# Performance work log

Measured on AMD Instinct MI355X. Metric: run time of the kernel, lower is better.

The kernel has to match this reference:

```python
import jax, jax.numpy as jnp
import numpy as np

MID = 16
HEADS = 8
HEAD_DIM = MID // HEADS  # 2
EPS = 1e-5


def posembed(length, dim):
    # get_posembed_linear: sin-cos 1D positional embedding
    pos = jnp.arange(length, dtype=jnp.float32)
    omega = jnp.arange(dim // 2, dtype=jnp.float32) / (dim / 2.0)
    omega = 1.0 / (10000.0 ** omega)
    out = pos[:, None] * omega[None, :]  # [L, dim//2]
    return jnp.concatenate([jnp.sin(out), jnp.cos(out)], axis=1)  # [L, dim]


def layernorm(x, g, b):
    m = x.mean(-1, keepdims=True)
    v = ((x - m) ** 2).mean(-1, keepdims=True)
    return (x - m) * jax.lax.rsqrt(v + EPS) * g + b


def conv2d(x, w, b):
    # NCHW 3x3 SAME conv
    y = jax.lax.conv_general_dilated(x, w, (1, 1), 'SAME',
                                     dimension_numbers=('NCHW', 'OIHW', 'NCHW'))
    return y + b[None, :, None, None]


def attention(x, wq, wk, wv, wo, bo):
    # diffusers Attention: self-attn, no qkv bias, out bias
    B, S, C = x.shape
    q = (x @ wq.T).reshape(B, S, HEADS, HEAD_DIM)
    k = (x @ wk.T).reshape(B, S, HEADS, HEAD_DIM)
    v = (x @ wv.T).reshape(B, S, HEADS, HEAD_DIM)
    scale = 1.0 / np.sqrt(HEAD_DIM).astype(np.float32)
    scores = jnp.einsum('bshd,bthd->bhst', q, k) * scale
    p = jax.nn.softmax(scores, axis=-1)
    o = jnp.einsum('bhst,bthd->bshd', p, v).reshape(B, S, C)
    return o @ wo.T + bo


def setup_inputs() -> dict:
    key = jax.random.key(0)
    ks = jax.random.split(key, 24)

    def n(k, shape, s=0.05):
        return jax.random.normal(k, shape, dtype=jnp.float32) * s

    b, f, h, w, c = 2, 16, 64, 64, 16
    inp = {
        'hidden_states': n(ks[0], (b, f, h, w, c), 1.0),
        'ref_stats': n(ks[1], (b, f, h, w, c), 1.0),
        'emb': n(ks[2], (b, 512), 1.0),
        'conv_in_w': n(ks[3], (MID, c, 3, 3)),
        'conv_in_b': jnp.zeros((MID,), jnp.float32),
        'emb1_w': n(ks[4], (MID, 512)),
        'emb1_b': jnp.zeros((MID,), jnp.float32),
        'emb2_w': n(ks[5], (MID, MID)),
        'emb2_b': jnp.zeros((MID,), jnp.float32),
        'wqx': n(ks[6], (MID, MID)), 'wkx': n(ks[7], (MID, MID)),
        'wvx': n(ks[8], (MID, MID)), 'wox': n(ks[9], (MID, MID)),
        'box': jnp.zeros((MID,), jnp.float32),
        'wqy': n(ks[10], (MID, MID)), 'wky': n(ks[11], (MID, MID)),
        'wvy': n(ks[12], (MID, MID)), 'woy': n(ks[13], (MID, MID)),
        'boy': jnp.zeros((MID,), jnp.float32),
        'wqt': n(ks[14], (MID, MID)), 'wkt': n(ks[15], (MID, MID)),
        'wvt': n(ks[16], (MID, MID)), 'wot': n(ks[17], (MID, MID)),
        'bot': jnp.zeros((MID,), jnp.float32),
        'norm_g': jnp.ones((MID,), jnp.float32),
        'norm_b': jnp.zeros((MID,), jnp.float32),
        'proj_w': n(ks[18], (c, MID, 3, 3)),  # zero_module in torch; random here so grads flow
        'proj_b': jnp.zeros((c,), jnp.float32),
    }
    return inp


def reference(hidden_states, ref_stats, emb,
              conv_in_w, conv_in_b, emb1_w, emb1_b, emb2_w, emb2_b,
              wqx, wkx, wvx, wox, box,
              wqy, wky, wvy, woy, boy,
              wqt, wkt, wvt, wot, bot,
              norm_g, norm_b, proj_w, proj_b):
    b, f, h, w, c = hidden_states.shape

    # conv stem on (b f) c h w
    x = hidden_states.reshape(b * f, h, w, c).transpose(0, 3, 1, 2)
    x = conv2d(x, conv_in_w, conv_in_b)
    r = ref_stats.reshape(b * f, h, w, c).transpose(0, 3, 1, 2)
    r = conv2d(r, conv_in_w, conv_in_b)

    # TimestepEmbedding: linear -> silu -> linear, broadcast over frames/HW
    e = jax.nn.silu(emb @ emb1_w.T + emb1_b) @ emb2_w.T + emb2_b  # [b, MID]
    r = r + jnp.repeat(e, f, axis=0)[:, :, None, None]

    hs = x.reshape(b, f, MID, h, w).transpose(0, 1, 3, 4, 2)  # b f h w c
    rs = r.reshape(b, f, MID, h, w).transpose(0, 1, 3, 4, 2)

    # row (x) attention: cat along w -> (b f h) 2w c
    cat = jnp.concatenate([hs, rs], axis=3).reshape(b * f * h, 2 * w, MID)
    pe = posembed(2 * w, MID)
    resx = attention(layernorm(cat + pe[None], norm_g, norm_b), wqx, wkx, wvx, wox, box)
    resx = resx[:, :w].reshape(b, f, h, w, MID)

    # column (y) attention: cat along h -> (b f w) 2h c
    cat = jnp.concatenate([resx, rs], axis=2)            # b f 2h w c
    cat = cat.transpose(0, 1, 3, 2, 4).reshape(b * f * w, 2 * h, MID)
    pe = posembed(2 * h, MID)
    resy = attention(layernorm(cat + pe[None], norm_g, norm_b), wqy, wky, wvy, woy, boy)
    resy = resy[:, :h].reshape(b, f, w, h, MID).transpose(0, 1, 3, 2, 4)

    # temporal (t) attention: cat along f -> (b h w) 2f c
    cat = jnp.concatenate([resy, rs], axis=1)            # b 2f h w c
    cat = cat.transpose(0, 2, 3, 1, 4).reshape(b * h * w, 2 * f, MID)
    pe = posembed(2 * f, MID)
    rest = attention(layernorm(cat + pe[None], norm_g, norm_b), wqt, wkt, wvt, wot, bot)
    rest = rest[:, :f].reshape(b, h, w, f, MID).transpose(0, 3, 4, 1, 2).reshape(b * f, MID, h, w)

    out = conv2d(rest, proj_w, proj_b)  # (b f) c h w
    return hidden_states + out.reshape(b, f, c, h, w).transpose(0, 1, 3, 4, 2)
```

## Files before the change

kernel.cpp:

```cpp
#include <hip/hip_runtime.h>
#include <hip/hip_bf16.h>

typedef __hip_bfloat16 bf16;
using hf2 = decltype(__builtin_amdgcn_cvt_pkrtz(0.f, 0.f));
typedef float f32x2 __attribute__((ext_vector_type(2)));

#define BB   2
#define FF   16
#define HH   64
#define WW   64
#define CC   16
#define NIMG (BB*FF)
#define PIX  (HH*WW)
#define IMGSZ (PIX*CC)

#define QSCALE_LOG2E 1.0201394f

__device__ __forceinline__ unsigned pkh2(float a, float b) {
    union { hf2 h; unsigned u; } x;
    x.h = __builtin_amdgcn_cvt_pkrtz(a, b);
    return x.u;
}
__device__ __forceinline__ float fdot2u(unsigned a, unsigned b, float c) {
    union { unsigned u; hf2 h; } A, B;
    A.u = a; B.u = b;
    return __builtin_amdgcn_fdot2(A.h, B.h, c, false);
}
__device__ __forceinline__ f32x2 f2(float a, float b) {
    f32x2 r; r.x = a; r.y = b; return r;
}

__device__ __forceinline__ void ld16bf(const bf16* p, float* x) {
    const uint4* p4 = reinterpret_cast<const uint4*>(p);
    uint4 u0 = p4[0], u1 = p4[1];
    unsigned uu[8] = {u0.x, u0.y, u0.z, u0.w, u1.x, u1.y, u1.z, u1.w};
    #pragma unroll
    for (int k = 0; k < 8; ++k) {
        union { unsigned u; float f; } lo, hi;
        lo.u = uu[k] << 16;
        hi.u = uu[k] & 0xffff0000u;
        x[2 * k] = lo.f;
        x[2 * k + 1] = hi.f;
    }
}
__device__ __forceinline__ void st16bf(bf16* p, const float* x) {
    union { bf16 h[16]; uint4 u[2]; } o;
    #pragma unroll
    for (int k = 0; k < 16; ++k) o.h[k] = __float2bfloat16(x[k]);
    uint4* p4 = reinterpret_cast<uint4*>(p);
    p4[0] = o.u[0];
    p4[1] = o.u[1];
}

__device__ __forceinline__ void ld16f(const float* p, float* x) {
    const float4* p4 = reinterpret_cast<const float4*>(p);
    #pragma unroll
    for (int q = 0; q < 4; ++q) {
        float4 v = p4[q];
        x[4 * q] = v.x; x[4 * q + 1] = v.y; x[4 * q + 2] = v.z; x[4 * q + 3] = v.w;
    }
}
__device__ __forceinline__ void st16f(float* p, const float* x) {
    float4* p4 = reinterpret_cast<float4*>(p);
    #pragma unroll
    for (int q = 0; q < 4; ++q)
        p4[q] = make_float4(x[4 * q], x[4 * q + 1], x[4 * q + 2], x[4 * q + 3]);
}

__device__ __forceinline__ unsigned packbf2(float a, float b) {
    union { bf16 h[2]; unsigned u; } pk;
    pk.h[0] = __float2bfloat16(a);
    pk.h[1] = __float2bfloat16(b);
    return pk.u;
}

__global__ __launch_bounds__(256) void conv_in_kernel(
    const float* __restrict__ hid, const float* __restrict__ ref,
    const float* __restrict__ cw, const float* __restrict__ cb,
    const float* __restrict__ emb,
    const float* __restrict__ e1w, const float* __restrict__ e1b,
    const float* __restrict__ e2w, const float* __restrict__ e2b,
    bf16* __restrict__ A, bf16* __restrict__ R)
{
    __shared__ unsigned w2l[9 * 128];
    __shared__ float bl[16], hl[16], el[16];
    __shared__ __align__(16) unsigned stg[6 * 64 * 10];

    int t = threadIdx.x;
    if (t < 128) {
        int oc = t & 15, c2 = t >> 4;
        #pragma unroll
        for (int k = 0; k < 9; ++k)
            w2l[k * 128 + oc * 8 + c2] =
                pkh2(cw[(oc * 16 + 2 * c2) * 9 + k],
                     cw[(oc * 16 + 2 * c2 + 1) * 9 + k]);
    }
    if (t < 16) bl[t] = cb[t];

    int gid  = blockIdx.x * 256 + t;
    int wi   = gid & 63;
    int hi   = (gid >> 6) & 63;
    int r0   = hi & ~3;
    int img2 = gid >> 12;
    int isref = img2 >> 5;
    int img  = img2 & 31;
    int bi   = img >> 4;

    if (isref) {
        float* red = reinterpret_cast<float*>(stg);
        {
            int o = t >> 4, seg = t & 15;
            const float* er = emb + bi * 512 + seg * 32;
            const float* wr = e1w + o * 512 + seg * 32;
            float p = 0.f;
            #pragma unroll
            for (int k = 0; k < 32; ++k) p = fmaf(er[k], wr[k], p);
            red[t] = p;
        }
        __syncthreads();
        if (t < 16) {
            float acc = e1b[t];
            #pragma unroll
            for (int s = 0; s < 16; ++s) acc += red[t * 16 + s];
            hl[t] = acc / (1.f + __expf(-acc));
        }
        __syncthreads();
        if (t < 16) {
            float acc = e2b[t];
            #pragma unroll
            for (int k = 0; k < 16; ++k) acc = fmaf(hl[k], e2w[t * 16 + k], acc);
            el[t] = acc;
        }
        __syncthreads();
    }

    const float* inp = (isref ? ref : hid) + (size_t)img * IMGSZ;
    #pragma unroll
    for (int pass = 0; pass < 2; ++pass) {
        int s = t + pass * 256;
        if (s < 384) {
            int px = s & 63, rr = s >> 6;
            int y  = r0 - 1 + rr;
            if ((unsigned)y < 64u) {
                float xv[16];
                ld16f(inp + (((y << 6) + px) << 4), xv);
                uint2* dst = reinterpret_cast<uint2*>(&stg[(rr * 64 + px) * 10]);
                #pragma unroll
                for (int e = 0; e < 4; ++e)
                    dst[e] = make_uint2(pkh2(xv[4 * e],     xv[4 * e + 1]),
                                        pkh2(xv[4 * e + 2], xv[4 * e + 3]));
            }
        }
    }
    __syncthreads();

    int rb = hi & 3;
    float acc[16];
    #pragma unroll
    for (int oc = 0; oc < 16; ++oc)
        acc[oc] = bl[oc] + (isref ? el[oc] : 0.f);

    #pragma unroll
    for (int ky = 0; ky < 3; ++ky) {
        int y = hi + ky - 1;
        if ((unsigned)y >= 64u) continue;
        int rr = rb + ky;
        #pragma unroll
        for (int kx = 0; kx < 3; ++kx) {
            int xx = wi + kx - 1;
            if ((unsigned)xx >= 64u) continue;
            const uint2* pp = reinterpret_cast<const uint2*>(&stg[(rr * 64 + xx) * 10]);
            uint2 p0 = pp[0], p1 = pp[1], p2 = pp[2], p3 = pp[3];
            unsigned xp[8] = {p0.x, p0.y, p1.x, p1.y, p2.x, p2.y, p3.x, p3.y};
            const unsigned* wt = &w2l[(ky * 3 + kx) * 128];
            #pragma unroll
            for (int oc = 0; oc < 16; ++oc) {
                float a = acc[oc];
                #pragma unroll
                for (int c2 = 0; c2 < 8; ++c2)
                    a = fdot2u(xp[c2], wt[oc * 8 + c2], a);
                acc[oc] = a;
            }
        }
    }
    bf16* op = (isref ? R : A) + ((size_t)(img * PIX + (hi << 6) + wi) << 4);
    st16bf(op, acc);
}

template<int S, int SEQPB, int MINW, bool F16OUT>
__global__ __launch_bounds__(256, MINW) void attn_kernel(
    bf16* __restrict__ A, const bf16* __restrict__ R,
    unsigned* __restrict__ A16,
    int d2, int str1, int str2, int tokStride,
    const float* __restrict__ wq, const float* __restrict__ wk,
    const float* __restrict__ wv, const float* __restrict__ wo,
    const float* __restrict__ bo, const float* __restrict__ gw,
    const float* __restrict__ bw)
{
    constexpr int HS  = S / 2;
    constexpr int KQ  = S / 2;
    constexpr int TPT = 256 / (SEQPB * S);
    constexpr int ITEMS = 256 / SEQPB;
    constexpr int NQG = ITEMS / 16;
    constexpr int QB  = HS / NQG;
    constexpr int QP  = QB / 2;
    constexpr int KROW = 10;
    constexpr int QROW = 20;
    constexpr int LSQ = (SEQPB == 1) ? 0 : ((SEQPB == 2) ? 1 : 2);
    constexpr int NW3 = SEQPB * HS * 8 / 256;

    __shared__ float wolT[256];
    __shared__ unsigned wq2L[128], wk2L[128], wv2L[128];
    __shared__ float bol[16], gl[16], blw[16];
    __shared__ __align__(16) unsigned kU[SEQPB * S * KROW];
    __shared__ __align__(16) unsigned vU[SEQPB * S * KROW];
    __shared__ __align__(16) unsigned qL[SEQPB * HS * KROW];
    __shared__ int bases[SEQPB];

    int t = threadIdx.x;
    wolT[(t & 15) * 16 + (t >> 4)] = wo[t];
    if (t < 128) {
        float2 qw = reinterpret_cast<const float2*>(wq)[t];
        float2 kw = reinterpret_cast<const float2*>(wk)[t];
        float2 vw = reinterpret_cast<const float2*>(wv)[t];
        wq2L[t] = pkh2(qw.x * QSCALE_LOG2E, qw.y * QSCALE_LOG2E);
        wk2L[t] = pkh2(kw.x, kw.y);
        wv2L[t] = pkh2(vw.x, vw.y);
    }
    if (t < 16) { bol[t] = bo[t]; gl[t] = gw[t]; blw[t] = bw[t]; }
    if (t < SEQPB) {
        int seq = blockIdx.x * SEQPB + t;
        bases[t] = (seq / d2) * str1 + (seq % d2) * str2;
    }
    __syncthreads();

    const float om[8] = {1.f, 0.31622776601683794f, 0.1f, 0.031622776601683794f,
                         0.01f, 0.0031622776601683794f, 0.001f, 0.00031622776601683794f};

    if constexpr (TPT == 2) {
        int tokIdx = t >> 1;
        int half = t & 1;
        int db   = half * 8;
        int sq = tokIdx & (SEQPB - 1);
        int i  = tokIdx >> LSQ;
        const bf16* src = ((i < HS)
            ? (A + bases[sq] + (size_t)i * tokStride)
            : (R + bases[sq] + (size_t)(i - HS) * tokStride)) + db;
        uint4 u = *reinterpret_cast<const uint4*>(src);
        unsigned uu[4] = {u.x, u.y, u.z, u.w};
        float x[8];
        #pragma unroll
        for (int k = 0; k < 4; ++k) {
            union { unsigned u; float f; } lo, hi2;
            lo.u = uu[k] << 16; hi2.u = uu[k] & 0xffff0000u;
            x[2 * k] = lo.f; x[2 * k + 1] = hi2.f;
        }
        float fi = (float)i;
        #pragma unroll
        for (int k = 0; k < 8; ++k) {
            float sv, cv;
            __sincosf(fi * om[k], &sv, &cv);
            x[k] += half ? cv : sv;
        }
        float s8 = 0.f;
        #pragma unroll
        for (int k = 0; k < 8; ++k) s8 += x[k];
        float m = (s8 + __shfl_xor(s8, 1)) * (1.f / 16.f);
        float v8 = 0.f;
        #pragma unroll
        for (int k = 0; k < 8; ++k) { float d = x[k] - m; v8 = fmaf(d, d, v8); }
        float var = (v8 + __shfl_xor(v8, 1)) * (1.f / 16.f);
        float rs = rsqrtf(var + 1e-5f);

        unsigned xpm[4];
        #pragma unroll
        for (int e = 0; e < 4; ++e) {
            float a0 = (x[2 * e]     - m) * rs * gl[db + 2 * e]     + blw[db + 2 * e];
            float a1 = (x[2 * e + 1] - m) * rs * gl[db + 2 * e + 1] + blw[db + 2 * e + 1];
            xpm[e] = pkh2(a0, a1);
        }
        unsigned xp[8];
        #pragma unroll
        for (int e = 0; e < 4; ++e) {
            unsigned oth = __shfl_xor(xpm[e], 1);
            xp[e]     = half ? oth    : xpm[e];
            xp[e + 4] = half ? xpm[e] : oth;
        }
        float qv[8], kv[8], vv[8];
        #pragma unroll
        for (int dd = 0; dd < 8; ++dd) {
            int d = db + dd;
            float aq = 0.f, ak = 0.f, av = 0.f;
            #pragma unroll
            for (int c2 = 0; c2 < 8; ++c2) {
                aq = fdot2u(xp[c2], wq2L[d * 8 + c2], aq);
                ak = fdot2u(xp[c2], wk2L[d * 8 + c2], ak);
                av = fdot2u(xp[c2], wv2L[d * 8 + c2], av);
            }
            qv[dd] = aq; kv[dd] = ak; vv[dd] = av;
        }
        int row = (sq * S + i) * KROW + (db >> 1);
        uint2* kr = reinterpret_cast<uint2*>(&kU[row]);
        uint2* vr = reinterpret_cast<uint2*>(&vU[row]);
        #pragma unroll
        for (int e = 0; e < 2; ++e) {
            kr[e] = make_uint2(pkh2(kv[4 * e], kv[4 * e + 1]),
                               pkh2(kv[4 * e + 2], kv[4 * e + 3]));
            vr[e] = make_uint2(packbf2(vv[4 * e], vv[4 * e + 1]),
                               packbf2(vv[4 * e + 2], vv[4 * e + 3]));
        }
        if (i < HS) {
            uint2* qr = reinterpret_cast<uint2*>(&qL[(sq * HS + i) * KROW + (db >> 1)]);
            #pragma unroll
            for (int e = 0; e < 2; ++e)
                qr[e] = make_uint2(pkh2(qv[4 * e], qv[4 * e + 1]),
                                   pkh2(qv[4 * e + 2], qv[4 * e + 3]));
        }
    } else {
        int sq = t & (SEQPB - 1);
        int i  = t >> LSQ;
        const bf16* src = (i < HS)
            ? (A + bases[sq] + (size_t)i * tokStride)
            : (R + bases[sq] + (size_t)(i - HS) * tokStride);
        float x[16];
        ld16bf(src, x);
        float fi = (float)i;
        #pragma unroll
        for (int k = 0; k < 8; ++k) {
            float sv, cv;
            __sincosf(fi * om[k], &sv, &cv);
            x[k]     += sv;
            x[k + 8] += cv;
        }
        float m = 0.f;
        #pragma unroll
        for (int c = 0; c < 16; ++c) m += x[c];
        m *= (1.f / 16.f);
        float var = 0.f;
        #pragma unroll
        for (int c = 0; c < 16; ++c) { float d = x[c] - m; var = fmaf(d, d, var); }
        var *= (1.f / 16.f);
        float rs = rsqrtf(var + 1e-5f);
        float xn[16];
        #pragma unroll
        for (int c = 0; c < 16; ++c) xn[c] = (x[c] - m) * rs * gl[c] + blw[c];

        unsigned xp[8];
        #pragma unroll
        for (int c2 = 0; c2 < 8; ++c2) xp[c2] = pkh2(xn[2 * c2], xn[2 * c2 + 1]);

        float qv[16], kv[16], vv[16];
        #pragma unroll
        for (int dd = 0; dd < 16; ++dd) {
            float aq = 0.f, ak = 0.f, av = 0.f;
            #pragma unroll
            for (int c2 = 0; c2 < 8; ++c2) {
                aq = fdot2u(xp[c2], wq2L[dd * 8 + c2], aq);
                ak = fdot2u(xp[c2], wk2L[dd * 8 + c2], ak);
                av = fdot2u(xp[c2], wv2L[dd * 8 + c2], av);
            }
            qv[dd] = aq; kv[dd] = ak; vv[dd] = av;
        }
        int row = (sq * S + i) * KROW;
        uint2* kr = reinterpret_cast<uint2*>(&kU[row]);
        uint2* vr = reinterpret_cast<uint2*>(&vU[row]);
        #pragma unroll
        for (int e = 0; e < 4; ++e) {
            kr[e] = make_uint2(pkh2(kv[4 * e], kv[4 * e + 1]),
                               pkh2(kv[4 * e + 2], kv[4 * e + 3]));
            vr[e] = make_uint2(packbf2(vv[4 * e], vv[4 * e + 1]),
                               packbf2(vv[4 * e + 2], vv[4 * e + 3]));
        }
        if (i < HS) {
            uint2* qr = reinterpret_cast<uint2*>(&qL[(sq * HS + i) * KROW]);
            #pragma unroll
            for (int e = 0; e < 4; ++e)
                qr[e] = make_uint2(pkh2(qv[4 * e], qv[4 * e + 1]),
                                   pkh2(qv[4 * e + 2], qv[4 * e + 3]));
        }
    }
    __syncthreads();

    int sq2 = t / ITEMS;
    int r   = t % ITEMS;
    int qg  = r >> 4;
    int hd  = (r >> 1) & 7;
    int half2 = r & 1;
    float* oL = reinterpret_cast<float*>(kU);
    {
        unsigned q2[QB];
        f32x2 l2[QP], a0p[QP], a1p[QP];
        #pragma unroll
        for (int qq = 0; qq < QB; ++qq)
            q2[qq] = qL[(sq2 * HS + qg * QB + qq) * KROW + hd];
        #pragma unroll
        for (int m = 0; m < QP; ++m) {
            l2[m] = f2(0.f, 0.f); a0p[m] = f2(0.f, 0.f); a1p[m] = f2(0.f, 0.f);
        }
        const unsigned* kp = &kU[(sq2 * S + half2) * KROW + hd];
        const unsigned* vp = &vU[(sq2 * S + half2) * KROW + hd];
        #pragma unroll 8
        for (int jj = 0; jj < KQ; ++jj) {
            unsigned ku = kp[jj * 2 * KROW];
            unsigned vu = vp[jj * 2 * KROW];
            union { unsigned u; float f; } v0, v1;
            v0.u = vu << 16; v1.u = vu & 0xffff0000u;
            f32x2 v00 = f2(v0.f, v0.f);
            f32x2 v11 = f2(v1.f, v1.f);
            #pragma unroll
            for (int m = 0; m < QP; ++m) {
                f32x2 p2;
                p2.x = __builtin_amdgcn_exp2f(fdot2u(q2[2 * m], ku, 0.f));
                p2.y = __builtin_amdgcn_exp2f(fdot2u(q2[2 * m + 1], ku, 0.f));
                l2[m] += p2;
                a0p[m] = __builtin_elementwise_fma(p2, v00, a0p[m]);
                a1p[m] = __builtin_elementwise_fma(p2, v11, a1p[m]);
            }
        }
        #pragma unroll
        for (int m = 0; m < QP; ++m) {
            l2[m].x  += __shfl_xor(l2[m].x, 1);  l2[m].y  += __shfl_xor(l2[m].y, 1);
            a0p[m].x += __shfl_xor(a0p[m].x, 1); a0p[m].y += __shfl_xor(a0p[m].y, 1);
            a1p[m].x += __shfl_xor(a1p[m].x, 1); a1p[m].y += __shfl_xor(a1p[m].y, 1);
        }
        __syncthreads();
        if (half2 == 0) {
            #pragma unroll
            for (int m = 0; m < QP; ++m) {
                float inv0 = 1.f / l2[m].x;
                float inv1 = 1.f / l2[m].y;
                *reinterpret_cast<float2*>(
                    &oL[(sq2 * HS + qg * QB + 2 * m) * QROW + 2 * hd]) =
                    make_float2(a0p[m].x * inv0, a1p[m].x * inv0);
                *reinterpret_cast<float2*>(
                    &oL[(sq2 * HS + qg * QB + 2 * m + 1) * QROW + 2 * hd]) =
                    make_float2(a0p[m].y * inv1, a1p[m].y * inv1);
            }
        }
    }
    __syncthreads();

    #pragma unroll
    for (int rep = 0; rep < NW3; ++rep) {
        int idx = t + rep * 256;
        int cp  = idx & 7;
        int g   = idx >> 3;
        int sq3 = g & (SEQPB - 1);
        int tok = g >> LSQ;
        const float* orow = &oL[(sq3 * HS + tok) * QROW];
        float acc0 = bol[2 * cp], acc1 = bol[2 * cp + 1];
        #pragma unroll
        for (int d = 0; d < 16; ++d) {
            acc0 = fmaf(orow[d], wolT[d * 16 + 2 * cp], acc0);
            acc1 = fmaf(orow[d], wolT[d * 16 + 2 * cp + 1], acc1);
        }
        int off = bases[sq3] + tok * tokStride;
        *reinterpret_cast<unsigned*>(A + off + 2 * cp) = packbf2(acc0, acc1);
        if constexpr (F16OUT)
            A16[(off >> 1) + cp] = pkh2(acc0, acc1);
    }
}

__global__ __launch_bounds__(256) void conv_out_kernel(
    const unsigned* __restrict__ A16, const float* __restrict__ hid,
    const float* __restrict__ pw, const float* __restrict__ pb,
    float* __restrict__ out)
{
    __shared__ unsigned w2l[9 * 128];
    __shared__ float bl[16];
    __shared__ __align__(16) unsigned stg[6 * 64 * 10];

    int t = threadIdx.x;
    if (t < 128) {
        int oc = t & 15, c2 = t >> 4;
        #pragma unroll
        for (int k = 0; k < 9; ++k)
            w2l[k * 128 + oc * 8 + c2] =
                pkh2(pw[(oc * 16 + 2 * c2) * 9 + k],
                     pw[(oc * 16 + 2 * c2 + 1) * 9 + k]);
    }
    if (t < 16) bl[t] = pb[t];

    int gid = blockIdx.x * 256 + t;
    int wi = gid & 63, hi = (gid >> 6) & 63;
    int r0 = hi & ~3;
    int img = gid >> 12;
    const unsigned* inp = A16 + ((size_t)img << 15);

    #pragma unroll
    for (int pass = 0; pass < 2; ++pass) {
        int s = t + pass * 256;
        if (s < 384) {
            int px = s & 63, rr = s >> 6;
            int y  = r0 - 1 + rr;
            if ((unsigned)y < 64u) {
                const uint4* sp = reinterpret_cast<const uint4*>(
                    inp + (((y << 6) + px) << 3));
                uint4 u0 = sp[0], u1 = sp[1];
                uint2* dst = reinterpret_cast<uint2*>(&stg[(rr * 64 + px) * 10]);
                dst[0] = make_uint2(u0.x, u0.y);
                dst[1] = make_uint2(u0.z, u0.w);
                dst[2] = make_uint2(u1.x, u1.y);
                dst[3] = make_uint2(u1.z, u1.w);
            }
        }
    }
    __syncthreads();

    int rb = hi & 3;
    float acc[16];
    #pragma unroll
    for (int oc = 0; oc < 16; ++oc) acc[oc] = bl[oc];

    #pragma unroll
    for (int ky = 0; ky < 3; ++ky) {
        int y = hi + ky - 1;
        if ((unsigned)y >= 64u) continue;
        int rr = rb + ky;
        #pragma unroll
        for (int kx = 0; kx < 3; ++kx) {
            int xx = wi + kx - 1;
            if ((unsigned)xx >= 64u) continue;
            const uint2* pp = reinterpret_cast<const uint2*>(&stg[(rr * 64 + xx) * 10]);
            uint2 p0 = pp[0], p1 = pp[1], p2 = pp[2], p3 = pp[3];
            unsigned xp[8] = {p0.x, p0.y, p1.x, p1.y, p2.x, p2.y, p3.x, p3.y};
            const unsigned* wt = &w2l[(ky * 3 + kx) * 128];
            #pragma unroll
            for (int oc = 0; oc < 16; ++oc) {
                float a = acc[oc];
                #pragma unroll
                for (int c2 = 0; c2 < 8; ++c2)
                    a = fdot2u(xp[c2], wt[oc * 8 + c2], a);
                acc[oc] = a;
            }
        }
    }
    size_t off = ((size_t)gid) << 4;
    float hv[16];
    ld16f(hid + off, hv);
    float res[16];
    #pragma unroll
    for (int k = 0; k < 16; ++k) res[k] = acc[k] + hv[k];
    st16f(out + off, res);
}

extern "C" void kernel_launch(void* const* d_in, const int* in_sizes, int n_in,
                              void* d_out, int out_size, void* d_ws, size_t ws_size,
                              hipStream_t stream) {
    const float* hid  = (const float*)d_in[0];
    const float* ref  = (const float*)d_in[1];
    const float* emb  = (const float*)d_in[2];
    const float* ciw  = (const float*)d_in[3];
    const float* cib  = (const float*)d_in[4];
    const float* e1w  = (const float*)d_in[5];
    const float* e1b  = (const float*)d_in[6];
    const float* e2w  = (const float*)d_in[7];
    const float* e2b  = (const float*)d_in[8];
    const float* wqx  = (const float*)d_in[9];
    const float* wkx  = (const float*)d_in[10];
    const float* wvx  = (const float*)d_in[11];
    const float* wox  = (const float*)d_in[12];
    const float* box_ = (const float*)d_in[13];
    const float* wqy  = (const float*)d_in[14];
    const float* wky  = (const float*)d_in[15];
    const float* wvy  = (const float*)d_in[16];
    const float* woy  = (const float*)d_in[17];
    const float* boy  = (const float*)d_in[18];
    const float* wqt  = (const float*)d_in[19];
    const float* wkt  = (const float*)d_in[20];
    const float* wvt  = (const float*)d_in[21];
    const float* wot  = (const float*)d_in[22];
    const float* bot  = (const float*)d_in[23];
    const float* ng   = (const float*)d_in[24];
    const float* nb   = (const float*)d_in[25];
    const float* pjw  = (const float*)d_in[26];
    const float* pjb  = (const float*)d_in[27];

    bf16* A = (bf16*)d_ws;
    unsigned* A16 = (unsigned*)((char*)d_ws + (4 << 20));
    bf16* R = (bf16*)d_out;

    conv_in_kernel<<<(2 * NIMG * PIX) / 256, 256, 0, stream>>>(
        hid, ref, ciw, cib, emb, e1w, e1b, e2w, e2b, A, R);

    attn_kernel<128, 1, 8, false><<<BB * FF * HH, 256, 0, stream>>>(
        A, R, nullptr, 1, WW * CC, 0, CC, wqx, wkx, wvx, wox, box_, ng, nb);
    attn_kernel<128, 2, 4, false><<<(BB * FF * WW) / 2, 256, 0, stream>>>(
        A, R, nullptr, WW, IMGSZ, CC, WW * CC, wqy, wky, wvy, woy, boy, ng, nb);
    attn_kernel<32, 4, 8, true><<<(BB * HH * WW) / 4, 256, 0, stream>>>(
        A, R, A16, HH * WW, FF * IMGSZ, CC, IMGSZ, wqt, wkt, wvt, wot, bot, ng, nb);

    conv_out_kernel<<<(NIMG * PIX) / 256, 256, 0, stream>>>(A16, hid, pjw, pjb, (float*)d_out);
}
```

Measured before the change: 233.2 us.

## Rewrite 3x3 convolutions with MFMA f16 matrix ops and padded LDS tiles

Both conv_in and conv_out replace the per-pixel scalar fdot2 loop with 16x16x16 f16 MFMA instructions over a zero-padded 66-wide LDS tile. Weights are staged per tap in B-operand layout. Each block now covers whole rows of 16-pixel groups. The y-attention launch changes to one sequence per block at higher occupancy, and the temporal attention skips the redundant bf16 store when it writes f16 output. Output stores are now scalar, strided per channel, which may hurt coalescing.

```diff
diff --git a/kernel.cpp b/kernel.cpp
--- a/kernel.cpp
+++ b/kernel.cpp
@@ -4,6 +4,8 @@
 typedef __hip_bfloat16 bf16;
 using hf2 = decltype(__builtin_amdgcn_cvt_pkrtz(0.f, 0.f));
 typedef float f32x2 __attribute__((ext_vector_type(2)));
+typedef _Float16 v4h __attribute__((ext_vector_type(4)));
+typedef float v4f __attribute__((ext_vector_type(4)));
 
 #define BB   2
 #define FF   16
@@ -43,14 +45,6 @@
         x[2 * k + 1] = hi.f;
     }
 }
-__device__ __forceinline__ void st16bf(bf16* p, const float* x) {
-    union { bf16 h[16]; uint4 u[2]; } o;
-    #pragma unroll
-    for (int k = 0; k < 16; ++k) o.h[k] = __float2bfloat16(x[k]);
-    uint4* p4 = reinterpret_cast<uint4*>(p);
-    p4[0] = o.u[0];
-    p4[1] = o.u[1];
-}
 
 __device__ __forceinline__ void ld16f(const float* p, float* x) {
     const float4* p4 = reinterpret_cast<const float4*>(p);
@@ -59,12 +53,6 @@
         float4 v = p4[q];
         x[4 * q] = v.x; x[4 * q + 1] = v.y; x[4 * q + 2] = v.z; x[4 * q + 3] = v.w;
     }
-}
-__device__ __forceinline__ void st16f(float* p, const float* x) {
-    float4* p4 = reinterpret_cast<float4*>(p);
-    #pragma unroll
-    for (int q = 0; q < 4; ++q)
-        p4[q] = make_float4(x[4 * q], x[4 * q + 1], x[4 * q + 2], x[4 * q + 3]);
 }
 
 __device__ __forceinline__ unsigned packbf2(float a, float b) {
@@ -73,6 +61,20 @@
     pk.h[1] = __float2bfloat16(b);
     return pk.u;
 }
+
+__device__ __forceinline__ void stage_wB(const float* __restrict__ w,
+                                         unsigned* __restrict__ wB, int t) {
+    for (int e = t; e < 576; e += 256) {
+        int oc = e & 15;
+        int c  = (e >> 4) & 3;
+        int s  = e >> 6;
+        const float* wp = w + (oc * 16 + c * 4) * 9 + s;
+        wB[e * 2]     = pkh2(wp[0],  wp[9]);
+        wB[e * 2 + 1] = pkh2(wp[18], wp[27]);
+    }
+}
+
+#define TAP_OFF(s) ((((s) / 3) * 66 + ((s) % 3)) * 12)
 
 __global__ __launch_bounds__(256) void conv_in_kernel(
     const float* __restrict__ hid, const float* __restrict__ ref,
@@ -82,29 +84,21 @@
     const float* __restrict__ e2w, const float* __restrict__ e2b,
     bf16* __restrict__ A, bf16* __restrict__ R)
 {
-    __shared__ unsigned w2l[9 * 128];
+    __shared__ __align__(16) unsigned stg[6 * 66 * 12];
+    __shared__ __align__(16) unsigned wB[1152];
     __shared__ float bl[16], hl[16], el[16];
-    __shared__ __align__(16) unsigned stg[6 * 64 * 10];
 
     int t = threadIdx.x;
-    if (t < 128) {
-        int oc = t & 15, c2 = t >> 4;
-        #pragma unroll
-        for (int k = 0; k < 9; ++k)
-            w2l[k * 128 + oc * 8 + c2] =
-                pkh2(cw[(oc * 16 + 2 * c2) * 9 + k],
-                     cw[(oc * 16 + 2 * c2 + 1) * 9 + k]);
-    }
+    int bid = blockIdx.x;
+    int rg   = bid & 15;
+    int img2 = bid >> 4;
+    int isref = img2 >> 5;
+    int img   = img2 & 31;
+    int bi    = img >> 4;
+    int r0    = rg << 2;
+
+    stage_wB(cw, wB, t);
     if (t < 16) bl[t] = cb[t];
-
-    int gid  = blockIdx.x * 256 + t;
-    int wi   = gid & 63;
-    int hi   = (gid >> 6) & 63;
-    int r0   = hi & ~3;
-    int img2 = gid >> 12;
-    int isref = img2 >> 5;
-    int img  = img2 & 31;
-    int bi   = img >> 4;
 
     if (isref) {
         float* red = reinterpret_cast<float*>(stg);
@@ -135,56 +129,54 @@
     }
 
     const float* inp = (isref ? ref : hid) + (size_t)img * IMGSZ;
-    #pragma unroll
-    for (int pass = 0; pass < 2; ++pass) {
-        int s = t + pass * 256;
-        if (s < 384) {
-            int px = s & 63, rr = s >> 6;
-            int y  = r0 - 1 + rr;
-            if ((unsigned)y < 64u) {
-                float xv[16];
-                ld16f(inp + (((y << 6) + px) << 4), xv);
-                uint2* dst = reinterpret_cast<uint2*>(&stg[(rr * 64 + px) * 10]);
-                #pragma unroll
-                for (int e = 0; e < 4; ++e)
-                    dst[e] = make_uint2(pkh2(xv[4 * e],     xv[4 * e + 1]),
-                                        pkh2(xv[4 * e + 2], xv[4 * e + 3]));
-            }
+    for (int s2 = t; s2 < 396; s2 += 256) {
+        int rr = s2 / 66, xi = s2 - rr * 66;
+        int y = r0 - 1 + rr, px = xi - 1;
+        uint4* dst = reinterpret_cast<uint4*>(&stg[(rr * 66 + xi) * 12]);
+        if ((unsigned)y < 64u && (unsigned)px < 64u) {
+            float xv[16];
+            ld16f(inp + (((y << 6) + px) << 4), xv);
+            dst[0] = make_uint4(pkh2(xv[0], xv[1]),  pkh2(xv[2], xv[3]),
+                                pkh2(xv[4], xv[5]),  pkh2(xv[6], xv[7]));
+            dst[1] = make_uint4(pkh2(xv[8], xv[9]),  pkh2(xv[10], xv[11]),
+                                pkh2(xv[12], xv[13]), pkh2(xv[14], xv[15]));
+        } else {
+            dst[0] = make_uint4(0, 0, 0, 0);
+            dst[1] = make_uint4(0, 0, 0, 0);
         }
     }
     __syncthreads();
 
-    int rb = hi & 3;
-    float acc[16];
-    #pragma unroll
-    for (int oc = 0; oc < 16; ++oc)
-        acc[oc] = bl[oc] + (isref ? el[oc] : 0.f);
-
-    #pragma unroll
-    for (int ky = 0; ky < 3; ++ky) {
-        int y = hi + ky - 1;
-        if ((unsigned)y >= 64u) continue;
-        int rr = rb + ky;
-        #pragma unroll
-        for (int kx = 0; kx < 3; ++kx) {
-            int xx = wi + kx - 1;
-            if ((unsigned)xx >= 64u) continue;
-            const uint2* pp = reinterpret_cast<const uint2*>(&stg[(rr * 64 + xx) * 10]);
-            uint2 p0 = pp[0], p1 = pp[1], p2 = pp[2], p3 = pp[3];
-            unsigned xp[8] = {p0.x, p0.y, p1.x, p1.y, p2.x, p2.y, p3.x, p3.y};
-            const unsigned* wt = &w2l[(ky * 3 + kx) * 128];
-            #pragma unroll
-            for (int oc = 0; oc < 16; ++oc) {
-                float a = acc[oc];
-                #pragma unroll
-                for (int c2 = 0; c2 < 8; ++c2)
-                    a = fdot2u(xp[c2], wt[oc * 8 + c2], a);
-                acc[oc] = a;
-            }
-        }
-    }
-    bf16* op = (isref ? R : A) + ((size_t)(img * PIX + (hi << 6) + wi) << 4);
-    st16bf(op, acc);
+    int l  = t & 63, w = t >> 6;
+    int oc = l & 15, c = l >> 4;
+    int y  = r0 + w;
+
+    v4h bf[9];
+    int cb2 = c * 32 + oc * 2;
+    #pragma unroll
+    for (int s = 0; s < 9; ++s)
+        bf[s] = *reinterpret_cast<const v4h*>(&wB[s * 128 + cb2]);
+
+    float bias = bl[oc] + (isref ? el[oc] : 0.f);
+    v4f binit; binit[0] = bias; binit[1] = bias; binit[2] = bias; binit[3] = bias;
+
+    bf16* op = (isref ? R : A) + (size_t)img * IMGSZ;
+
+    #pragma unroll
+    for (int xq = 0; xq < 4; ++xq) {
+        int ab = (w * 66 + xq * 16 + (l & 15)) * 12 + 2 * c;
+        v4f acc = binit;
+        #pragma unroll
+        for (int s = 0; s < 9; ++s) {
+            v4h af = *reinterpret_cast<const v4h*>(&stg[ab + TAP_OFF(s)]);
+            acc = __builtin_amdgcn_mfma_f32_16x16x16f16(af, bf[s], acc, 0, 0, 0);
+        }
+        #pragma unroll
+        for (int g = 0; g < 4; ++g) {
+            int x = xq * 16 + c * 4 + g;
+            op[(((y << 6) + x) << 4) + oc] = __float2bfloat16(acc[g]);
+        }
+    }
 }
 
 template<int S, int SEQPB, int MINW, bool F16OUT>
@@ -455,9 +447,10 @@
             acc1 = fmaf(orow[d], wolT[d * 16 + 2 * cp + 1], acc1);
         }
         int off = bases[sq3] + tok * tokStride;
-        *reinterpret_cast<unsigned*>(A + off + 2 * cp) = packbf2(acc0, acc1);
         if constexpr (F16OUT)
             A16[(off >> 1) + cp] = pkh2(acc0, acc1);
+        else
+            *reinterpret_cast<unsigned*>(A + off + 2 * cp) = packbf2(acc0, acc1);
     }
 }
 
@@ -466,82 +459,68 @@
     const float* __restrict__ pw, const float* __restrict__ pb,
     float* __restrict__ out)
 {
-    __shared__ unsigned w2l[9 * 128];
+    __shared__ __align__(16) unsigned stg[4 * 66 * 12];
+    __shared__ __align__(16) unsigned wB[1152];
     __shared__ float bl[16];
-    __shared__ __align__(16) unsigned stg[6 * 64 * 10];
 
     int t = threadIdx.x;
-    if (t < 128) {
-        int oc = t & 15, c2 = t >> 4;
-        #pragma unroll
-        for (int k = 0; k < 9; ++k)
-            w2l[k * 128 + oc * 8 + c2] =
-                pkh2(pw[(oc * 16 + 2 * c2) * 9 + k],
-                     pw[(oc * 16 + 2 * c2 + 1) * 9 + k]);
-    }
+    int bid = blockIdx.x;
+    int rg  = bid & 31;
+    int img = bid >> 5;
+    int r0  = rg << 1;
+
+    stage_wB(pw, wB, t);
     if (t < 16) bl[t] = pb[t];
 
-    int gid = blockIdx.x * 256 + t;
-    int wi = gid & 63, hi = (gid >> 6) & 63;
-    int r0 = hi & ~3;
-    int img = gid >> 12;
     const unsigned* inp = A16 + ((size_t)img << 15);
-
-    #pragma unroll
-    for (int pass = 0; pass < 2; ++pass) {
-        int s = t + pass * 256;
-        if (s < 384) {
-            int px = s & 63, rr = s >> 6;
-            int y  = r0 - 1 + rr;
-            if ((unsigned)y < 64u) {
-                const uint4* sp = reinterpret_cast<const uint4*>(
-                    inp + (((y << 6) + px) << 3));
-                uint4 u0 = sp[0], u1 = sp[1];
-                uint2* dst = reinterpret_cast<uint2*>(&stg[(rr * 64 + px) * 10]);
-                dst[0] = make_uint2(u0.x, u0.y);
-                dst[1] = make_uint2(u0.z, u0.w);
-                dst[2] = make_uint2(u1.x, u1.y);
-                dst[3] = make_uint2(u1.z, u1.w);
-            }
+    for (int s2 = t; s2 < 264; s2 += 256) {
+        int rr = s2 / 66, xi = s2 - rr * 66;
+        int y = r0 - 1 + rr, px = xi - 1;
+        uint4* dst = reinterpret_cast<uint4*>(&stg[(rr * 66 + xi) * 12]);
+        if ((unsigned)y < 64u && (unsigned)px < 64u) {
+            const uint4* sp = reinterpret_cast<const uint4*>(
+                inp + (((y << 6) + px) << 3));
+            dst[0] = sp[0];
+            dst[1] = sp[1];
+        } else {
+            dst[0] = make_uint4(0, 0, 0, 0);
+            dst[1] = make_uint4(0, 0, 0, 0);
         }
     }
     __syncthreads();
 
-    int rb = hi & 3;
-    float acc[16];
-    #pragma unroll
-    for (int oc = 0; oc < 16; ++oc) acc[oc] = bl[oc];
-
-    #pragma unroll
-    for (int ky = 0; ky < 3; ++ky) {
-        int y = hi + ky - 1;
-        if ((unsigned)y >= 64u) continue;
-        int rr = rb + ky;
-        #pragma unroll
-        for (int kx = 0; kx < 3; ++kx) {
-            int xx = wi + kx - 1;
-            if ((unsigned)xx >= 64u) continue;
-            const uint2* pp = reinterpret_cast<const uint2*>(&stg[(rr * 64 + xx) * 10]);
-            uint2 p0 = pp[0], p1 = pp[1], p2 = pp[2], p3 = pp[3];
-            unsigned xp[8] = {p0.x, p0.y, p1.x, p1.y, p2.x, p2.y, p3.x, p3.y};
-            const unsigned* wt = &w2l[(ky * 3 + kx) * 128];
-            #pragma unroll
-            for (int oc = 0; oc < 16; ++oc) {
-                float a = acc[oc];
-                #pragma unroll
-                for (int c2 = 0; c2 < 8; ++c2)
-                    a = fdot2u(xp[c2], wt[oc * 8 + c2], a);
-                acc[oc] = a;
-            }
-        }
-    }
-    size_t off = ((size_t)gid) << 4;
-    float hv[16];
-    ld16f(hid + off, hv);
-    float res[16];
-    #pragma unroll
-    for (int k = 0; k < 16; ++k) res[k] = acc[k] + hv[k];
-    st16f(out + off, res);
+    int l  = t & 63, w = t >> 6;
+    int oc = l & 15, c = l >> 4;
+
+    v4h bf[9];
+    int cb2 = c * 32 + oc * 2;
+    #pragma unroll
+    for (int s = 0; s < 9; ++s)
+        bf[s] = *reinterpret_cast<const v4h*>(&wB[s * 128 + cb2]);
+
+    float bias = bl[oc];
+    v4f binit; binit[0] = bias; binit[1] = bias; binit[2] = bias; binit[3] = bias;
+    size_t obase = (size_t)img * IMGSZ;
+
+    #pragma unroll
+    for (int tq = 0; tq < 2; ++tq) {
+        int tile = w * 2 + tq;
+        int ro = tile >> 2, xq = tile & 3;
+        int y  = r0 + ro;
+        int ab = (ro * 66 + xq * 16 + (l & 15)) * 12 + 2 * c;
+        v4f acc = binit;
+        #pragma unroll
+        for (int s = 0; s < 9; ++s) {
+            v4h af = *reinterpret_cast<const v4h*>(&stg[ab + TAP_OFF(s)]);
+            acc = __builtin_amdgcn_mfma_f32_16x16x16f16(af, bf[s], acc, 0, 0, 0);
+        }
+        #pragma unroll
+        for (int g = 0; g < 4; ++g) {
+            int x = xq * 16 + c * 4 + g;
+            size_t o = obase + (size_t)(((y << 6) + x) << 4) + oc;
+            out[o] = acc[g] + hid[o];
+        }
+    }
 }
 
 extern "C" void kernel_launch(void* const* d_in, const int* in_sizes, int n_in,
@@ -580,15 +559,16 @@
     unsigned* A16 = (unsigned*)((char*)d_ws + (4 << 20));
     bf16* R = (bf16*)d_out;
 
-    conv_in_kernel<<<(2 * NIMG * PIX) / 256, 256, 0, stream>>>(
+    conv_in_kernel<<<2 * NIMG * (HH / 4), 256, 0, stream>>>(
         hid, ref, ciw, cib, emb, e1w, e1b, e2w, e2b, A, R);
 
     attn_kernel<128, 1, 8, false><<<BB * FF * HH, 256, 0, stream>>>(
         A, R, nullptr, 1, WW * CC, 0, CC, wqx, wkx, wvx, wox, box_, ng, nb);
-    attn_kernel<128, 2, 4, false><<<(BB * FF * WW) / 2, 256, 0, stream>>>(
+    attn_kernel<128, 1, 8, false><<<BB * FF * WW, 256, 0, stream>>>(
         A, R, nullptr, WW, IMGSZ, CC, WW * CC, wqy, wky, wvy, woy, boy, ng, nb);
     attn_kernel<32, 4, 8, true><<<(BB * HH * WW) / 4, 256, 0, stream>>>(
         A, R, A16, HH * WW, FF * IMGSZ, CC, IMGSZ, wqt, wkt, wvt, wot, bot, ng, nb);
 
-    conv_out_kernel<<<(NIMG * PIX) / 256, 256, 0, stream>>>(A16, hid, pjw, pjb, (float*)d_out);
-}
+    conv_out_kernel<<<NIMG * (HH / 2), 256, 0, stream>>>(
+        A16, hid, pjw, pjb, (float*)d_out);
+}
```

After: 224.0 us. -4.0%, faster.
